# Kernel tuning notes

Hardware: AMD Instinct MI355X
Metric: run time of the kernel (lower is better)

Reference implementation:

```python
import jax, jax.numpy as jnp
import numpy as np

B, S, D_MODEL, D_K, D_V = 8, 2048, 1024, 1024, 1024


def setup_inputs() -> dict:
    key = jax.random.key(0)
    ks = jax.random.split(key, 10)
    scale = 1.0 / np.sqrt(D_MODEL)
    return {
        "inputs_q": jax.random.normal(ks[0], (B, S, D_MODEL), dtype=jnp.float32),
        "inputs_k": jax.random.normal(ks[1], (B, S, D_MODEL), dtype=jnp.float32),
        "inputs_v": jax.random.normal(ks[2], (B, S, D_MODEL), dtype=jnp.float32),
        "mask": jax.random.randint(ks[3], (B, S), 0, 2, dtype=jnp.int32),
        "Wq": jax.random.normal(ks[4], (D_MODEL, D_K), dtype=jnp.float32) * scale,
        "bq": jnp.zeros((D_K,), dtype=jnp.float32),
        "Wk": jax.random.normal(ks[5], (D_MODEL, D_K), dtype=jnp.float32) * scale,
        "bk": jnp.zeros((D_K,), dtype=jnp.float32),
        "Wv": jax.random.normal(ks[6], (D_MODEL, D_V), dtype=jnp.float32) * scale,
        "bv": jnp.zeros((D_V,), dtype=jnp.float32),
    }


def reference(inputs_q, inputs_k, inputs_v, mask, Wq, bq, Wk, bk, Wv, bv):
    # Dense projections: [B,S,d_model] @ [d_model,d] + bias
    q = jnp.einsum("bsd,dk->bsk", inputs_q, Wq) + bq
    k = jnp.einsum("bsd,dk->bsk", inputs_k, Wk) + bk
    v = jnp.einsum("bsd,dv->bsv", inputs_v, Wv) + bv
    # scaled dot-product scores [B,S,S]
    scores = jnp.einsum("bqk,bsk->bqs", q, k) / jnp.sqrt(jnp.float32(D_K))
    # padding mask [B,S] -> matrix mask via min(row, col); 1 = valid
    m = mask.astype(jnp.float32)
    matrix_mask = jnp.minimum(m[:, :, None], m[:, None, :])  # [B,S,S]
    mask_float = 1.0 - matrix_mask  # 1 where masked
    scores = scores + mask_float * (-1e9)
    attention_weights = jax.nn.softmax(scores, axis=-1)
    out = jnp.einsum("bqs,bsv->bqv", attention_weights, v)  # [B,S,d_v]
    return out
```

## Files before the change

kernel.cpp:

```cpp
#include <hip/hip_runtime.h>
#include <stdint.h>


typedef unsigned short u16;
typedef __attribute__((ext_vector_type(8))) short short8;
typedef __attribute__((ext_vector_type(4))) float f32x4;

__device__ __forceinline__ u16 f2bf(float x) {
  unsigned u = __float_as_uint(x);
  return (u16)((u + 0x7FFFu + ((u >> 16) & 1u)) >> 16);
}
__device__ __forceinline__ float bf2f(u16 h) {
  return __uint_as_float(((unsigned)h) << 16);
}

__device__ __forceinline__ void stage16(const void* g, void* l) {
  const __attribute__((address_space(1))) uint32_t* gp =
      (const __attribute__((address_space(1))) uint32_t*)(uintptr_t)g;
  __attribute__((address_space(3))) uint32_t* lp =
      (__attribute__((address_space(3))) uint32_t*)(uintptr_t)l;
  __builtin_amdgcn_global_load_lds(gp, lp, 16, 0, 0);
}

__device__ __forceinline__ short8 ld8(const char* p, int off) {
  return *(const short8*)(p + off);
}

__global__ __launch_bounds__(256) void scanwt(const int* __restrict__ mask,
                                              int* __restrict__ idxA,
                                              int* __restrict__ nvA,
                                              int* __restrict__ nvp128A,
                                              const float* __restrict__ Wq,
                                              const float* __restrict__ Wk,
                                              const float* __restrict__ Wv,
                                              u16* __restrict__ WT,
                                              const float* __restrict__ Xv,
                                              float* __restrict__ partial) {
  __shared__ int wsum[4];
  __shared__ float tile[32][33];
  const int bid = blockIdx.x;
  const int t = threadIdx.x;
  if (bid < 8) {
    const int b = bid;
    const int lane = t & 63, w = t >> 6;
    const int* m = mask + b * 2048;
    int v[8], loc = 0;
#pragma unroll
    for (int i = 0; i < 8; ++i) { v[i] = m[t * 8 + i]; loc += v[i]; }
    int sc = loc;
    for (int off = 1; off < 64; off <<= 1) {
      int n = __shfl_up(sc, off);
      if (lane >= off) sc += n;
    }
    if (lane == 63) wsum[w] = sc;
    __syncthreads();
    int woff = 0;
    for (int i = 0; i < w; ++i) woff += wsum[i];
    int pos = woff + sc - loc;
#pragma unroll
    for (int i = 0; i < 8; ++i)
      if (v[i]) idxA[b * 2048 + (pos++)] = t * 8 + i;
    if (t == 255) {
      const int nv = woff + sc;
      nvA[b] = nv;
      nvp128A[b] = (nv + 127) & ~127;
    }
  } else if (bid < 3080) {
    const int q = bid - 8;
    const int z = q >> 10;
    const int xy = q & 1023;
    const int n0 = (xy & 31) * 32, d0 = (xy >> 5) * 32;
    const float* W = (z == 0) ? Wq : (z == 1) ? Wk : Wv;
    u16* out = WT + (size_t)z * 1024 * 1024;
    const int tx = t & 31, ty = t >> 5;
#pragma unroll
    for (int i = 0; i < 4; ++i)
      tile[ty + 8 * i][tx] = W[(size_t)(d0 + ty + 8 * i) * 1024 + n0 + tx];
    __syncthreads();
#pragma unroll
    for (int i = 0; i < 4; ++i)
      out[(size_t)(n0 + ty + 8 * i) * 1024 + d0 + tx] = f2bf(tile[tx][ty + 8 * i]);
  } else {
    const int r = bid - 3080;
    const int b = r & 7, dq = (r >> 3) & 3, sck = r >> 5;
    const int d = dq * 256 + t;
    const float* p = Xv + ((size_t)b * 2048 + sck * 256) * 1024 + d;
    float s0 = 0, s1 = 0, s2 = 0, s3 = 0;
    for (int rr = 0; rr < 256; rr += 4) {
      s0 += p[(size_t)(rr + 0) * 1024];
      s1 += p[(size_t)(rr + 1) * 1024];
      s2 += p[(size_t)(rr + 2) * 1024];
      s3 += p[(size_t)(rr + 3) * 1024];
    }
    partial[((size_t)b * 8 + sck) * 1024 + d] = (s0 + s1) + (s2 + s3);
  }
}

__global__ __launch_bounds__(256) void compact3(const float* __restrict__ Xq,
                                                const float* __restrict__ Xk,
                                                const float* __restrict__ Xv,
                                                const int* __restrict__ idxA,
                                                const int* __restrict__ nvA,
                                                u16* __restrict__ Oq,
                                                u16* __restrict__ Ok,
                                                u16* __restrict__ Ov) {
  const int b = blockIdx.y, z = blockIdx.z;
  const int w = threadIdx.x >> 6, lane = threadIdx.x & 63;
  const int j = blockIdx.x * 4 + w;
  if (j >= nvA[b]) return;
  const float* X = (z == 0) ? Xq : (z == 1) ? Xk : Xv;
  u16* out = (z == 0) ? Oq : (z == 1) ? Ok : Ov;
  const int src = idxA[b * 2048 + j];
  const float4* s = (const float4*)(X + ((size_t)b * 2048 + src) * 1024);
  ushort4* d = (ushort4*)(out + ((size_t)b * 2048 + j) * 1024);
#pragma unroll
  for (int p = 0; p < 4; ++p) {
    const float4 f = s[lane + p * 64];
    ushort4 o;
    o.x = f2bf(f.x); o.y = f2bf(f.y); o.z = f2bf(f.z); o.w = f2bf(f.w);
    d[lane + p * 64] = o;
  }
}

#define BAR __builtin_amdgcn_s_barrier()
#define SB __builtin_amdgcn_sched_barrier(0)
#define LGK0 asm volatile("s_waitcnt lgkmcnt(0)" ::: "memory")
#define VM4 asm volatile("s_waitcnt vmcnt(4)" ::: "memory")
#define VM0 asm volatile("s_waitcnt vmcnt(0)" ::: "memory")

#define RDA4(P0, P1, MH)                                      \
  {                                                           \
    _Pragma("unroll") for (int mf_ = 0; mf_ < 4; ++mf_) {     \
      afr[0][mf_] = ld8(P0, (MH) * 8192 + mf_ * 2048);        \
      afr[1][mf_] = ld8(P1, (MH) * 8192 + mf_ * 2048);        \
    }                                                         \
  }

#define RDB2(DST, P0, P1, NH)                                 \
  {                                                           \
    DST[0][0] = ld8(P0, (NH) * 4096);                         \
    DST[0][1] = ld8(P0, (NH) * 4096 + 2048);                  \
    DST[1][0] = ld8(P1, (NH) * 4096);                         \
    DST[1][1] = ld8(P1, (NH) * 4096 + 2048);                  \
  }

#define MQ16(ACC, NH, BF)                                                \
  __builtin_amdgcn_s_setprio(1);                                         \
  {                                                                      \
    _Pragma("unroll") for (int ks_ = 0; ks_ < 2; ++ks_)                  \
        _Pragma("unroll") for (int mf_ = 0; mf_ < 4; ++mf_)              \
            _Pragma("unroll") for (int nf_ = 0; nf_ < 2; ++nf_)          \
                ACC[mf_][(NH) * 2 + nf_] =                               \
                    __builtin_amdgcn_mfma_f32_16x16x32_bf16(             \
                        afr[ks_][mf_], BF[ks_][nf_],                     \
                        ACC[mf_][(NH) * 2 + nf_], 0, 0, 0);              \
  }                                                                      \
  __builtin_amdgcn_s_setprio(0);

__global__ __launch_bounds__(512, 2) void gemm8p(
    const u16* __restrict__ A, const u16* __restrict__ B,
    void* __restrict__ C, void* __restrict__ C1, void* __restrict__ C2,
    const float* __restrict__ b0, const float* __restrict__ b1,
    const float* __restrict__ b2,
    const int* __restrict__ nvp128A,
    const float* __restrict__ partial, const float* __restrict__ WvF,
    float* __restrict__ vpart,
    int K, int lda, int ldb, int ldc) {
  __shared__ __attribute__((aligned(16))) char smem[131072];

  if (blockIdx.x >= 768) {
    float* mx = (float*)smem;
    const int r2 = blockIdx.x - 768;
    const int b = r2 & 7, cq = (r2 >> 3) & 1, dk = r2 >> 4;
    const int t = threadIdx.x;
    if (t < 128) {
      const int d = dk * 128 + t;
      float m = 0;
#pragma unroll
      for (int i = 0; i < 8; ++i) m += partial[((size_t)b * 8 + i) * 1024 + d];
      mx[t] = m * (1.0f / 2048.0f);
    }
    __syncthreads();
    const int c = cq * 512 + t;
    const float* wp = WvF + (size_t)(dk * 128) * 1024 + c;
    float acc = 0;
#pragma unroll 4
    for (int i = 0; i < 128; ++i) acc += mx[i] * wp[(size_t)i * 1024];
    vpart[((size_t)b * 8 + dk) * 1024 + c] = acc;
    return;
  }

  const int tid = threadIdx.x;
  const int lane = tid & 63;
  const int w = tid >> 6;
  const int wr = w >> 2;
  const int wc = w & 3;

  const int bx = blockIdx.x;
  const int z = bx & 7;
  int r = bx >> 3;
  const int o = r >> 5; r &= 31;
  const int bm = r >> 2, bn = r & 3;

  const int nvp = nvp128A[z];
  if (bm * 256 >= nvp) return;

  const u16* Ap = A + (size_t)o * (8u * 2048u * 1024u) + (size_t)z * (2048u * 1024u);
  const u16* Bp = B + (size_t)o * (1024u * 1024u);
  const int half = K >> 7;

  const int srow = w * 8 + (lane >> 3);
  const int scol = ((lane & 7) ^ (lane >> 3)) << 3;
  const u16* Ab0 = Ap + (size_t)(bm * 256 + srow) * lda + scol;
  const u16* Ab1 = Ab0 + (size_t)64 * lda;
  const u16* Ab2 = Ab0 + (size_t)128 * lda;
  const u16* Ab3 = Ab0 + (size_t)192 * lda;
  const u16* Bb0 = Bp + (size_t)(bn * 256 + srow) * ldb + scol;
  const u16* Bb1 = Bb0 + (size_t)64 * ldb;
  const u16* Bb2 = Bb0 + (size_t)128 * ldb;
  const u16* Bb3 = Bb0 + (size_t)192 * ldb;
  char* ldsW = smem + w * 1024;

  const int fr = lane & 15;
  const int fq = lane >> 4;
  const int fx = (fr & 7) << 4;
  const char* pak0 = smem + wr * 16384 + fr * 128 + ((fq * 16) ^ fx);
  const char* pak1 = smem + wr * 16384 + fr * 128 + ((64 + fq * 16) ^ fx);
  const char* pak0b = pak0 + 65536;
  const char* pak1b = pak1 + 65536;
  const char* pbk0 = smem + 32768 + wc * 8192 + fr * 128 + ((fq * 16) ^ fx);
  const char* pbk1 = smem + 32768 + wc * 8192 + fr * 128 + ((64 + fq * 16) ^ fx);
  const char* pbk0b = pbk0 + 65536;
  const char* pbk1b = pbk1 + 65536;

  f32x4 acc0[4][4] = {};
  f32x4 acc1[4][4] = {};
  short8 afr[2][4], bf0[2][2], bf1[2][2];

  stage16(Bb0, ldsW + 32768); stage16(Bb1, ldsW + 40960);
  stage16(Bb2, ldsW + 49152); stage16(Bb3, ldsW + 57344);
  stage16(Ab0, ldsW + 0);     stage16(Ab1, ldsW + 8192);
  stage16(Ab2, ldsW + 16384); stage16(Ab3, ldsW + 24576);
  stage16(Bb0 + 64, ldsW + 98304);  stage16(Bb1 + 64, ldsW + 106496);
  stage16(Bb2 + 64, ldsW + 114688); stage16(Bb3 + 64, ldsW + 122880);
  VM4;
  BAR;

  int koff = 0;
  for (int i = 0; i < half - 1; ++i) {
    const int o1 = koff + 64, o2 = koff + 128, o3 = koff + 192;
    RDA4(pak0, pak1, 0); RDB2(bf0, pbk0, pbk1, 0);
    stage16(Ab0 + o1, ldsW + 65536); stage16(Ab1 + o1, ldsW + 73728);
    SB; BAR; LGK0; MQ16(acc0, 0, bf0); BAR;
    RDB2(bf1, pbk0, pbk1, 1);
    stage16(Ab2 + o1, ldsW + 81920); stage16(Ab3 + o1, ldsW + 90112);
    SB; BAR; LGK0; MQ16(acc0, 1, bf1); BAR;
    RDA4(pak0, pak1, 1);
    stage16(Bb0 + o2, ldsW + 32768); stage16(Bb1 + o2, ldsW + 40960);
    SB; BAR; LGK0; MQ16(acc1, 0, bf0); BAR;
    stage16(Bb2 + o2, ldsW + 49152); stage16(Bb3 + o2, ldsW + 57344);
    SB; BAR; MQ16(acc1, 1, bf1); VM4; BAR;
    RDA4(pak0b, pak1b, 0); RDB2(bf0, pbk0b, pbk1b, 0);
    stage16(Ab0 + o2, ldsW + 0); stage16(Ab1 + o2, ldsW + 8192);
    SB; BAR; LGK0; MQ16(acc0, 0, bf0); BAR;
    RDB2(bf1, pbk0b, pbk1b, 1);
    stage16(Ab2 + o2, ldsW + 16384); stage16(Ab3 + o2, ldsW + 24576);
    SB; BAR; LGK0; MQ16(acc0, 1, bf1); BAR;
    RDA4(pak0b, pak1b, 1);
    stage16(Bb0 + o3, ldsW + 98304); stage16(Bb1 + o3, ldsW + 106496);
    SB; BAR; LGK0; MQ16(acc1, 0, bf0); BAR;
    stage16(Bb2 + o3, ldsW + 114688); stage16(Bb3 + o3, ldsW + 122880);
    SB; BAR; MQ16(acc1, 1, bf1); VM4; BAR;
    koff += 128;
  }
  {
    const int o1 = koff + 64;
    RDA4(pak0, pak1, 0); RDB2(bf0, pbk0, pbk1, 0);
    stage16(Ab0 + o1, ldsW + 65536); stage16(Ab1 + o1, ldsW + 73728);
    SB; BAR; LGK0; MQ16(acc0, 0, bf0); BAR;
    RDB2(bf1, pbk0, pbk1, 1);
    stage16(Ab2 + o1, ldsW + 81920); stage16(Ab3 + o1, ldsW + 90112);
    SB; BAR; LGK0; MQ16(acc0, 1, bf1); BAR;
    RDA4(pak0, pak1, 1);
    SB; BAR; LGK0; MQ16(acc1, 0, bf0); BAR;
    SB; BAR; MQ16(acc1, 1, bf1); VM0; BAR;
    RDA4(pak0b, pak1b, 0); RDB2(bf0, pbk0b, pbk1b, 0);
    SB; BAR; LGK0; MQ16(acc0, 0, bf0); BAR;
    RDB2(bf1, pbk0b, pbk1b, 1);
    SB; BAR; LGK0; MQ16(acc0, 1, bf1); BAR;
    RDA4(pak0b, pak1b, 1);
    SB; BAR; LGK0; MQ16(acc1, 0, bf0); BAR;
    SB; BAR; MQ16(acc1, 1, bf1); BAR;
  }

  const int colb = bn * 256 + wc * 64 + fr;
#pragma unroll
  for (int mh = 0; mh < 2; ++mh) {
    f32x4(&ac)[4][4] = mh ? acc1 : acc0;
    const int rowl = bm * 256 + wr * 128 + mh * 64 + fq * 4;
    if (o < 2) {
      const float* bp = o ? b1 : b0;
      u16* Cb = (u16*)(o ? C1 : C) + (size_t)z * (2048u * 1024u);
#pragma unroll
      for (int mf = 0; mf < 4; ++mf)
#pragma unroll
        for (int n = 0; n < 4; ++n) {
          const int c = colb + n * 16;
          const float bv = bp[c];
#pragma unroll
          for (int j = 0; j < 4; ++j)
            Cb[(size_t)(rowl + mf * 16 + j) * ldc + c] = f2bf(ac[mf][n][j] + bv);
        }
    } else {
      u16* Cb = (u16*)C2;
#pragma unroll
      for (int mf = 0; mf < 4; ++mf) {
        const int s_ = rowl + mf * 16;
#pragma unroll
        for (int n = 0; n < 4; ++n) {
          const int c = colb + n * 16;
          const float bv = b2[c];
          ushort4 ov;
          ov.x = f2bf(ac[mf][n][0] + bv);
          ov.y = f2bf(ac[mf][n][1] + bv);
          ov.z = f2bf(ac[mf][n][2] + bv);
          ov.w = f2bf(ac[mf][n][3] + bv);
          *(ushort4*)&Cb[((size_t)z * 1024 + c) * 2048 + s_] = ov;
        }
      }
    }
  }
}

template <int MODE>
__global__ __launch_bounds__(256, 2) void gemm128(
    const u16* __restrict__ A, const u16* __restrict__ B, void* __restrict__ C,
    const int* __restrict__ nvp128A, const int* __restrict__ nvA,
    const int* __restrict__ idxA,
    const float* __restrict__ p0, const float* __restrict__ p1,
    float* __restrict__ p2,
    int K, int lda, int ldb, int ldc,
    size_t Az, size_t Bz, size_t Cz) {
  __shared__ __attribute__((aligned(16))) u16 lsA[2 * 128 * 32];
  __shared__ __attribute__((aligned(16))) u16 lsB[2 * 128 * 32];

  if constexpr (MODE == 2) {
    if (blockIdx.x >= 2048) {
      const int r2 = blockIdx.x - 2048;
      const int b = r2 & 7, cq = r2 >> 3;
      const int c = cq * 256 + threadIdx.x;
      float acc = p1[c];
#pragma unroll
      for (int i = 0; i < 8; ++i) acc += p0[((size_t)b * 8 + i) * 1024 + c];
      p2[b * 1024 + c] = acc;
      return;
    }
  }

  const int tid = threadIdx.x;
  const int lane = tid & 63;
  const int w = tid >> 6;
  const int wr = w >> 1, wc = w & 1;

  const int bx = blockIdx.x;
  const int z = bx & 7;
  const int r = bx >> 3;
  int bm, bn;
  if constexpr (MODE == 2) { bm = r >> 4; bn = r & 15; }
  else                     { bm = r >> 3; bn = r & 7; }

  const int nvp = nvp128A[z];
  if (bm * 128 >= nvp) return;
  if constexpr (MODE == 2) { if (bn * 128 >= nvp) return; }
  const int Kz = (MODE == 3) ? nvp : K;

  const u16* Ap = A + (size_t)z * Az;
  const u16* Bp = B + (size_t)z * Bz;

  const int srow = lane >> 2;
  const int scol = (lane & 3) * 8;
  const u16* Ag0 = Ap + (size_t)(bm * 128 + w * 32 + srow) * lda + scol;
  const u16* Ag1 = Ag0 + (size_t)16 * lda;
  const u16* Bg0 = Bp + (size_t)(bn * 128 + w * 32 + srow) * ldb + scol;
  const u16* Bg1 = Bg0 + (size_t)16 * ldb;
  u16* lA0 = &lsA[(w * 32) * 32];
  u16* lA1 = &lsA[(w * 32 + 16) * 32];
  u16* lB0 = &lsB[(w * 32) * 32];
  u16* lB1 = &lsB[(w * 32 + 16) * 32];

  const int arow = wr * 64 + (lane & 15);
  const int brow = wc * 64 + (lane & 15);
  const int ko = (lane >> 4) * 8;

  f32x4 acc[4][4] = {};

  auto compute = [&](int cur) {
    const u16* sA = lsA + cur * 4096;
    const u16* sB = lsB + cur * 4096;
    short8 af[4], bfr[4];
#pragma unroll
    for (int m = 0; m < 4; ++m)
      af[m] = *(const short8*)&sA[(arow + m * 16) * 32 + ko];
#pragma unroll
    for (int n = 0; n < 4; ++n)
      bfr[n] = *(const short8*)&sB[(brow + n * 16) * 32 + ko];
#pragma unroll
    for (int m = 0; m < 4; ++m)
#pragma unroll
      for (int n = 0; n < 4; ++n)
        acc[m][n] =
            __builtin_amdgcn_mfma_f32_16x16x32_bf16(af[m], bfr[n], acc[m][n], 0, 0, 0);
  };

  stage16(Ag0, lA0);
  stage16(Ag1, lA1);
  stage16(Bg0, lB0);
  stage16(Bg1, lB1);
  __syncthreads();

  int cur = 0;
  int k0 = 0;
  for (; k0 + 32 < Kz; k0 += 32) {
    const int off = (cur ^ 1) * 4096;
    const int kn = k0 + 32;
    stage16(Ag0 + kn, lA0 + off);
    stage16(Ag1 + kn, lA1 + off);
    stage16(Bg0 + kn, lB0 + off);
    stage16(Bg1 + kn, lB1 + off);
    compute(cur);
    __syncthreads();
    cur ^= 1;
  }
  compute(cur);

  const int col0 = bn * 128 + wc * 64 + (lane & 15);
  const int row0 = bm * 128 + wr * 64 + ((lane >> 4) << 2);

  if constexpr (MODE == 2) {
    u16* Cb = (u16*)C + (size_t)z * Cz;
#pragma unroll
    for (int m = 0; m < 4; ++m)
#pragma unroll
      for (int n = 0; n < 4; ++n) {
        const int c = col0 + n * 16;
#pragma unroll
        for (int j = 0; j < 4; ++j)
          Cb[(size_t)(row0 + m * 16 + j) * ldc + c] =
              f2bf(acc[m][n][j] * 0.03125f);
      }
  } else {
    const int nv = nvA[z];
    const int* idxp = idxA + z * 2048;
    float* Ob = (float*)C;
#pragma unroll
    for (int m = 0; m < 4; ++m)
#pragma unroll
      for (int j = 0; j < 4; ++j) {
        const int rowc = row0 + m * 16 + j;
        if (rowc < nv) {
          const int gr = idxp[rowc];
          float* orow = Ob + ((size_t)z * 2048 + gr) * 1024;
#pragma unroll
          for (int n = 0; n < 4; ++n) orow[col0 + n * 16] = acc[m][n][j];
        }
      }
  }
}

__global__ __launch_bounds__(256) void softbc(u16* __restrict__ scores,
                                              const int* __restrict__ nvA,
                                              const int* __restrict__ nvp128A,
                                              const int* __restrict__ mask,
                                              const float* __restrict__ vmean,
                                              float* __restrict__ out) {
  const int b = blockIdx.y, row = blockIdx.x;
  if (blockIdx.z == 1) {
    if (mask[b * 2048 + row] != 0) return;
    const float4 vv = ((const float4*)(vmean + b * 1024))[threadIdx.x];
    ((float4*)(out + ((size_t)b * 2048 + row) * 1024))[threadIdx.x] = vv;
    return;
  }
  const int nv = nvA[b];
  if (row >= nv) return;
  const int nvp = nvp128A[b];
  const int t = threadIdx.x, lane = t & 63, w = t >> 6;
  u16* sc = scores + ((size_t)b * 2048 + row) * 2048;
  const int c0 = t * 8;
  float v[8];
  if (c0 < nvp) {
    const ushort4 h0 = *(const ushort4*)&sc[c0];
    const ushort4 h1 = *(const ushort4*)&sc[c0 + 4];
    v[0] = bf2f(h0.x); v[1] = bf2f(h0.y); v[2] = bf2f(h0.z); v[3] = bf2f(h0.w);
    v[4] = bf2f(h1.x); v[5] = bf2f(h1.y); v[6] = bf2f(h1.z); v[7] = bf2f(h1.w);
  } else {
#pragma unroll
    for (int i = 0; i < 8; ++i) v[i] = 0.f;
  }
  float lmax = -3.0e38f;
#pragma unroll
  for (int i = 0; i < 8; ++i)
    if (c0 + i < nv) lmax = fmaxf(lmax, v[i]);
#pragma unroll
  for (int off = 32; off >= 1; off >>= 1) lmax = fmaxf(lmax, __shfl_xor(lmax, off));
  __shared__ float red[8];
  if (lane == 0) red[w] = lmax;
  __syncthreads();
  const float bmax = fmaxf(fmaxf(red[0], red[1]), fmaxf(red[2], red[3]));
  float e[8];
  float lsum = 0.f;
#pragma unroll
  for (int i = 0; i < 8; ++i) {
    e[i] = (c0 + i < nv) ? __expf(v[i] - bmax) : 0.f;
    lsum += e[i];
  }
#pragma unroll
  for (int off = 32; off >= 1; off >>= 1) lsum += __shfl_xor(lsum, off);
  if (lane == 0) red[4 + w] = lsum;
  __syncthreads();
  const float inv = 1.0f / ((red[4] + red[5]) + (red[6] + red[7]));
  if (c0 < nvp) {
    ushort4 o0, o1;
    o0.x = f2bf(e[0] * inv); o0.y = f2bf(e[1] * inv);
    o0.z = f2bf(e[2] * inv); o0.w = f2bf(e[3] * inv);
    o1.x = f2bf(e[4] * inv); o1.y = f2bf(e[5] * inv);
    o1.z = f2bf(e[6] * inv); o1.w = f2bf(e[7] * inv);
    *(ushort4*)&sc[c0] = o0;
    *(ushort4*)&sc[c0 + 4] = o1;
  }
}

extern "C" void kernel_launch(void* const* d_in, const int* in_sizes, int n_in,
                              void* d_out, int out_size, void* d_ws, size_t ws_size,
                              hipStream_t stream) {
  const float* in_q = (const float*)d_in[0];
  const float* in_k = (const float*)d_in[1];
  const float* in_v = (const float*)d_in[2];
  const int* mask = (const int*)d_in[3];
  const float* Wq = (const float*)d_in[4];
  const float* bq = (const float*)d_in[5];
  const float* Wk = (const float*)d_in[6];
  const float* bk = (const float*)d_in[7];
  const float* Wv = (const float*)d_in[8];
  const float* bv = (const float*)d_in[9];

  char* ws = (char*)d_ws;
  const size_t SZ = (size_t)16384 * 1024 * 2;
  u16* qc = (u16*)(ws);
  u16* kc = (u16*)(ws + SZ);
  u16* vcT = (u16*)(ws + 2 * SZ);
  u16* Xc = (u16*)(ws + 3 * SZ);
  u16* Xqc = Xc;
  u16* Xkc = Xc + (size_t)8 * 2048 * 1024;
  u16* Xvc = Xkc + (size_t)8 * 2048 * 1024;
  u16* scores = (u16*)(ws + 3 * SZ);
  u16* WT = (u16*)(ws + 6 * SZ);
  char* misc = ws + 6 * SZ + 6 * 1024 * 1024;
  int* idxA = (int*)misc;
  int* nvA = idxA + 8 * 2048;
  int* nvp128A = nvA + 8;
  float* partial = (float*)(misc + 128 * 1024);
  float* vmean = (float*)(misc + 384 * 1024);
  float* vpart = (float*)(misc + 448 * 1024);

  scanwt<<<3336, 256, 0, stream>>>(mask, idxA, nvA, nvp128A, Wq, Wk, Wv, WT,
                                   in_v, partial);

  compact3<<<dim3(512, 8, 3), 256, 0, stream>>>(in_q, in_k, in_v, idxA, nvA,
                                                Xqc, Xkc, Xvc);

  gemm8p<<<896, 512, 0, stream>>>(
      Xqc, WT, qc, kc, vcT, bq, bk, bv, nvp128A, partial, Wv, vpart,
      1024, 1024, 1024, 1024);

  gemm128<2><<<2080, 256, 0, stream>>>(
      qc, kc, scores, nvp128A, nvA, idxA, vpart, bv, vmean,
      1024, 1024, 1024, 2048,
      (size_t)2048 * 1024, (size_t)2048 * 1024, (size_t)2048 * 2048);

  softbc<<<dim3(2048, 8, 2), 256, 0, stream>>>(scores, nvA, nvp128A, mask,
                                               vmean, (float*)d_out);

  gemm128<3><<<1024, 256, 0, stream>>>(
      scores, vcT, d_out, nvp128A, nvA, idxA, nullptr, nullptr, nullptr,
      0, 2048, 2048, 1024,
      (size_t)2048 * 2048, (size_t)1024 * 2048, 0);
}
```

Baseline: 230.6 us.

## Deepen K-tile to 64 with XOR-swizzled LDS layout in gemm128

Doubles the K step per pipeline stage from 32 to 64, so each iteration stages 128x64 tiles of A and B into a 64KB double buffer. Global-to-LDS column offsets are XOR-swizzled by row, and the MFMA fragment reads apply the matching swizzle to avoid LDS bank conflicts. This halves the number of barriers per K and reduces conflicts. In exchange it uses 64KB of LDS per block, which may limit occupancy under launch_bounds(256,2), and it assumes Kz is a multiple of 64.

```diff
diff --git a/kernel.cpp b/kernel.cpp
--- a/kernel.cpp
+++ b/kernel.cpp
@@ -341,8 +341,7 @@
     float* __restrict__ p2,
     int K, int lda, int ldb, int ldc,
     size_t Az, size_t Bz, size_t Cz) {
-  __shared__ __attribute__((aligned(16))) u16 lsA[2 * 128 * 32];
-  __shared__ __attribute__((aligned(16))) u16 lsB[2 * 128 * 32];
+  __shared__ __attribute__((aligned(16))) char smem[65536];
 
   if constexpr (MODE == 2) {
     if (blockIdx.x >= 2048) {
@@ -377,56 +376,59 @@
   const u16* Ap = A + (size_t)z * Az;
   const u16* Bp = B + (size_t)z * Bz;
 
-  const int srow = lane >> 2;
-  const int scol = (lane & 3) * 8;
-  const u16* Ag0 = Ap + (size_t)(bm * 128 + w * 32 + srow) * lda + scol;
-  const u16* Ag1 = Ag0 + (size_t)16 * lda;
-  const u16* Bg0 = Bp + (size_t)(bn * 128 + w * 32 + srow) * ldb + scol;
-  const u16* Bg1 = Bg0 + (size_t)16 * ldb;
-  u16* lA0 = &lsA[(w * 32) * 32];
-  u16* lA1 = &lsA[(w * 32 + 16) * 32];
-  u16* lB0 = &lsB[(w * 32) * 32];
-  u16* lB1 = &lsB[(w * 32 + 16) * 32];
-
-  const int arow = wr * 64 + (lane & 15);
-  const int brow = wc * 64 + (lane & 15);
-  const int ko = (lane >> 4) * 8;
+  const int sr8 = lane >> 3;
+  const int scolE = ((lane & 7) ^ sr8) << 3;
+  const u16* Ag = Ap + (size_t)(bm * 128 + w * 8 + sr8) * lda + scolE;
+  const u16* Bg = Bp + (size_t)(bn * 128 + w * 8 + sr8) * ldb + scolE;
+  char* ldsW = smem + w * 1024;
+
+  const int fr = lane & 15;
+  const int fq = lane >> 4;
+  const int fx = (fr & 7) << 4;
+  const int kx0 = (fq * 16) ^ fx;
+  const int kx1 = (64 + fq * 16) ^ fx;
 
   f32x4 acc[4][4] = {};
 
-  auto compute = [&](int cur) {
-    const u16* sA = lsA + cur * 4096;
-    const u16* sB = lsB + cur * 4096;
-    short8 af[4], bfr[4];
-#pragma unroll
-    for (int m = 0; m < 4; ++m)
-      af[m] = *(const short8*)&sA[(arow + m * 16) * 32 + ko];
-#pragma unroll
-    for (int n = 0; n < 4; ++n)
-      bfr[n] = *(const short8*)&sB[(brow + n * 16) * 32 + ko];
-#pragma unroll
-    for (int m = 0; m < 4; ++m)
+  auto stage = [&](int kt, int buf) {
+    char* base = ldsW + buf * 32768;
+#pragma unroll
+    for (int j = 0; j < 4; ++j)
+      stage16(Ag + (size_t)(j * 32) * lda + kt, base + j * 4096);
+#pragma unroll
+    for (int j = 0; j < 4; ++j)
+      stage16(Bg + (size_t)(j * 32) * ldb + kt, base + 16384 + j * 4096);
+  };
+
+  auto compute = [&](int buf) {
+    const char* sA = smem + buf * 32768;
+    const char* sB = sA + 16384;
+#pragma unroll
+    for (int ks = 0; ks < 2; ++ks) {
+      const int kx = ks ? kx1 : kx0;
+      short8 af[4], bfr[4];
+#pragma unroll
+      for (int m = 0; m < 4; ++m)
+        af[m] = *(const short8*)(sA + (wr * 64 + m * 16 + fr) * 128 + kx);
 #pragma unroll
       for (int n = 0; n < 4; ++n)
-        acc[m][n] =
-            __builtin_amdgcn_mfma_f32_16x16x32_bf16(af[m], bfr[n], acc[m][n], 0, 0, 0);
+        bfr[n] = *(const short8*)(sB + (wc * 64 + n * 16 + fr) * 128 + kx);
+#pragma unroll
+      for (int m = 0; m < 4; ++m)
+#pragma unroll
+        for (int n = 0; n < 4; ++n)
+          acc[m][n] = __builtin_amdgcn_mfma_f32_16x16x32_bf16(af[m], bfr[n],
+                                                              acc[m][n], 0, 0, 0);
+    }
   };
 
-  stage16(Ag0, lA0);
-  stage16(Ag1, lA1);
-  stage16(Bg0, lB0);
-  stage16(Bg1, lB1);
+  stage(0, 0);
   __syncthreads();
 
   int cur = 0;
   int k0 = 0;
-  for (; k0 + 32 < Kz; k0 += 32) {
-    const int off = (cur ^ 1) * 4096;
-    const int kn = k0 + 32;
-    stage16(Ag0 + kn, lA0 + off);
-    stage16(Ag1 + kn, lA1 + off);
-    stage16(Bg0 + kn, lB0 + off);
-    stage16(Bg1 + kn, lB1 + off);
+  for (; k0 + 64 < Kz; k0 += 64) {
+    stage(k0 + 64, cur ^ 1);
     compute(cur);
     __syncthreads();
     cur ^= 1;
```

Result: no change. 231.6 us (+0.4%).
